# Kernel tuning notes

Measured on AMD Instinct MI355X. Metric: run time of the kernel, lower is better.

## Reference

```python
import jax, jax.numpy as jnp
import numpy as np

EMBED = 384
HEADS = 6
HEAD_SIZE = EMBED // HEADS
EPS = 1e-5


def _layernorm(x, g, b):
    mu = jnp.mean(x, axis=-1, keepdims=True)
    var = jnp.mean(jnp.square(x - mu), axis=-1, keepdims=True)
    return (x - mu) * jax.lax.rsqrt(var + EPS) * g + b


def setup_inputs() -> dict:
    key = jax.random.key(0)
    ks = jax.random.split(key, 16)
    B, T = 64, 256
    s_in = 1.0 / np.sqrt(EMBED)
    return {
        "x": jax.random.normal(ks[0], (B, T, EMBED), dtype=jnp.float32),
        # per-head q/k/v projections, stacked over heads: [H, C, D]
        "Wq": jax.random.normal(ks[1], (HEADS, EMBED, HEAD_SIZE), dtype=jnp.float32) * s_in,
        "bq": jnp.zeros((HEADS, HEAD_SIZE), dtype=jnp.float32),
        "Wk": jax.random.normal(ks[2], (HEADS, EMBED, HEAD_SIZE), dtype=jnp.float32) * s_in,
        "bk": jnp.zeros((HEADS, HEAD_SIZE), dtype=jnp.float32),
        "Wv": jax.random.normal(ks[3], (HEADS, EMBED, HEAD_SIZE), dtype=jnp.float32) * s_in,
        "bv": jnp.zeros((HEADS, HEAD_SIZE), dtype=jnp.float32),
        "Wp": jax.random.normal(ks[4], (EMBED, EMBED), dtype=jnp.float32) * s_in,
        "bp": jnp.zeros((EMBED,), dtype=jnp.float32),
        "W1": jax.random.normal(ks[5], (EMBED, EMBED), dtype=jnp.float32) * s_in,
        "b1": jnp.zeros((EMBED,), dtype=jnp.float32),
        "W2": jax.random.normal(ks[6], (EMBED, EMBED), dtype=jnp.float32) * s_in,
        "b2": jnp.zeros((EMBED,), dtype=jnp.float32),
        "ln1_g": jnp.ones((EMBED,), dtype=jnp.float32),
        "ln1_b": jnp.zeros((EMBED,), dtype=jnp.float32),
        "ln2_g": jnp.ones((EMBED,), dtype=jnp.float32),
        "ln2_b": jnp.zeros((EMBED,), dtype=jnp.float32),
    }


def reference(x, Wq, bq, Wk, bk, Wv, bv, Wp, bp, W1, b1, W2, b2,
              ln1_g, ln1_b, ln2_g, ln2_b):
    B, T, C = x.shape
    h = _layernorm(x, ln1_g, ln1_b)
    # batched per-head projections: [B,H,T,D]
    q = jnp.einsum('btc,hcd->bhtd', h, Wq) + bq[None, :, None, :]
    k = jnp.einsum('btc,hcd->bhtd', h, Wk) + bk[None, :, None, :]
    v = jnp.einsum('btc,hcd->bhtd', h, Wv) + bv[None, :, None, :]
    # NOTE: original scales by embed_size**0.5 (C=384), not head_size.
    wei = jnp.einsum('bhtd,bhsd->bhts', q, k) / jnp.sqrt(jnp.float32(C))
    causal = jnp.tril(jnp.ones((T, T), dtype=bool))
    wei = jnp.where(causal[None, None], wei, -jnp.inf)
    wei = jax.nn.softmax(wei, axis=-1)  # dropout = identity in eval
    attn = jnp.einsum('bhts,bhsd->bhtd', wei, v)  # [B,H,T,D]
    # concat heads in head order -> [B,T,C]
    attn = attn.transpose(0, 2, 1, 3).reshape(B, T, C)
    x = x + attn @ Wp + bp
    h2 = _layernorm(x, ln2_g, ln2_b)
    ff = jax.nn.relu(h2 @ W1 + b1) @ W2 + b2
    return x + ff
```

## Files before the change

### kernel.cpp

```cpp
#include <hip/hip_runtime.h>

typedef _Float16 f16;
typedef _Float16 half8 __attribute__((ext_vector_type(8)));
typedef _Float16 half4v __attribute__((ext_vector_type(4)));
typedef float floatx4 __attribute__((ext_vector_type(4)));

#define B_ 64
#define T_ 256
#define C_ 384
#define H_ 6
#define D_ 64
#define NROWS (B_*T_)

typedef __attribute__((address_space(3))) void lds_void_t;
typedef const __attribute__((address_space(1))) void gvoid_t;

__device__ __forceinline__ void g2lds16(const void* g, void* l) {
  __builtin_amdgcn_global_load_lds((gvoid_t*)g, (lds_void_t*)l, 16, 0, 0);
}

__global__ __launch_bounds__(256) void prep_ln_kernel(
    const float* __restrict__ Wq, const float* __restrict__ Wk, const float* __restrict__ Wv,
    const float* __restrict__ bq, const float* __restrict__ bk, const float* __restrict__ bv,
    const float* __restrict__ Wp, const float* __restrict__ W1, const float* __restrict__ W2,
    f16* __restrict__ Wqkv_t, f16* __restrict__ Wp_t, f16* __restrict__ W1_t, f16* __restrict__ W2_t,
    float* __restrict__ bqkv,
    const float* __restrict__ x, const float* __restrict__ gamma, const float* __restrict__ beta,
    f16* __restrict__ hout)
{
  const int bid = blockIdx.x;
  const int tid = threadIdx.x;
  if (bid >= 217) {
    int row = (bid - 217) * 4 + (tid >> 6);
    int lane = tid & 63;
    const float* xr = x + (size_t)row * 384;
    float v[6]; float s = 0.f;
#pragma unroll
    for (int j = 0; j < 6; j++) { v[j] = xr[lane + 64*j]; s += v[j]; }
#pragma unroll
    for (int m = 1; m < 64; m <<= 1) s += __shfl_xor(s, m);
    float mu = s * (1.f/384.f);
    float var = 0.f;
#pragma unroll
    for (int j = 0; j < 6; j++) { float d = v[j]-mu; var += d*d; }
#pragma unroll
    for (int m = 1; m < 64; m <<= 1) var += __shfl_xor(var, m);
    float rs = rsqrtf(var * (1.f/384.f) + 1e-5f);
    f16* orow = hout + (size_t)row*384;
#pragma unroll
    for (int j = 0; j < 6; j++) {
      int col = lane + 64*j;
      orow[col] = (f16)((v[j]-mu)*rs*gamma[col] + beta[col]);
    }
    return;
  }
  if (bid == 216) {
    for (int i = tid; i < 1152; i += 256) {
      float v;
      if (i < 384)      v = bq[i];
      else if (i < 768) v = bk[i - 384];
      else              v = bv[i - 768];
      bqkv[i] = v;
    }
    return;
  }
  __shared__ __align__(16) float tile[64*68];
  const float* src; int srcStride; f16* dst;
  if (bid < 108) {
    int mat = bid / 36, rem = bid - mat*36;
    int h = rem / 6, kt = rem - h*6;
    const float* W = (mat == 0) ? Wq : (mat == 1) ? Wk : Wv;
    src = W + (size_t)(h*384 + kt*64)*64;
    srcStride = 64;
    dst = Wqkv_t + (size_t)(mat*384 + h*64)*384 + kt*64;
  } else {
    int b2 = bid - 108;
    int mat = b2 / 36, rem = b2 - mat*36;
    int kt = rem / 6, ct = rem - kt*6;
    const float* W = (mat == 0) ? Wp : (mat == 1) ? W1 : W2;
    src = W + (size_t)(kt*64)*384 + ct*64;
    srcStride = 384;
    f16* O = (mat == 0) ? Wp_t : (mat == 1) ? W1_t : W2_t;
    dst = O + (size_t)(ct*64)*384 + kt*64;
  }
#pragma unroll
  for (int i = 0; i < 4; i++) {
    int idx = i*256 + tid;
    int r = idx >> 4, c4 = idx & 15;
    float4 v = *(const float4*)(src + (size_t)r*srcStride + c4*4);
    *(float4*)(&tile[r*68 + c4*4]) = v;
  }
  __syncthreads();
#pragma unroll
  for (int i = 0; i < 4; i++) {
    int idx = i*256 + tid;
    int d = idx >> 4, k4 = idx & 15;
    half4v o;
#pragma unroll
    for (int j = 0; j < 4; j++) o[j] = (f16)tile[(k4*4 + j)*68 + d];
    *(half4v*)(dst + (size_t)d*384 + k4*4) = o;
  }
}

__global__ __launch_bounds__(256) void ln_kernel(const float* __restrict__ x,
    const float* __restrict__ gamma, const float* __restrict__ beta, f16* __restrict__ out)
{
  int row = blockIdx.x * 4 + (threadIdx.x >> 6);
  int lane = threadIdx.x & 63;
  const float* xr = x + (size_t)row * 384;
  float v[6]; float s = 0.f;
#pragma unroll
  for (int j = 0; j < 6; j++) { v[j] = xr[lane + 64*j]; s += v[j]; }
#pragma unroll
  for (int m = 1; m < 64; m <<= 1) s += __shfl_xor(s, m);
  float mu = s * (1.f/384.f);
  float var = 0.f;
#pragma unroll
  for (int j = 0; j < 6; j++) { float d = v[j]-mu; var += d*d; }
#pragma unroll
  for (int m = 1; m < 64; m <<= 1) var += __shfl_xor(var, m);
  float rs = rsqrtf(var * (1.f/384.f) + 1e-5f);
  f16* orow = out + (size_t)row*384;
#pragma unroll
  for (int j = 0; j < 6; j++) {
    int col = lane + 64*j;
    orow[col] = (f16)((v[j]-mu)*rs*gamma[col] + beta[col]);
  }
}

template<int MODE>
__global__ __launch_bounds__(256) void gemm_kernel(
    const f16* __restrict__ A, const f16* __restrict__ Bt,
    const float* __restrict__ bias, const float* __restrict__ res,
    void* __restrict__ outp, int ldo)
{
  __shared__ __align__(16) f16 As[2][128*32];
  __shared__ __align__(16) f16 Bs[2][128*32];
  const int tid = threadIdx.x;
  const int lane = tid & 63, w = tid >> 6;
  const int wm = w >> 1, wn = w & 1;
  const int q = lane >> 4, c15 = lane & 15;
  const long row0 = (long)blockIdx.x * 128;
  const long col0 = (long)blockIdx.y * 128;
  floatx4 acc[4][4] = {};

  const int c0 = tid,        r0c = c0 >> 2, p0 = c0 & 3, g0 = p0 ^ ((r0c >> 1) & 3);
  const int c1 = 256 + tid,  r1c = c1 >> 2, p1 = c1 & 3, g1 = p1 ^ ((r1c >> 1) & 3);
  const f16* Arow0 = A  + (row0 + r0c)*384 + g0*8;
  const f16* Arow1 = A  + (row0 + r1c)*384 + g1*8;
  const f16* Brow0 = Bt + (col0 + r0c)*384 + g0*8;
  const f16* Brow1 = Bt + (col0 + r1c)*384 + g1*8;
  const int dof0 = (w*64)*8, dof1 = (256 + w*64)*8;

  for (int k0 = 0; k0 < 384; k0 += 64) {
#pragma unroll
    for (int hf = 0; hf < 2; hf++) {
      int kk = k0 + hf*32;
      g2lds16(Arow0 + kk, &As[hf][dof0]);
      g2lds16(Arow1 + kk, &As[hf][dof1]);
      g2lds16(Brow0 + kk, &Bs[hf][dof0]);
      g2lds16(Brow1 + kk, &Bs[hf][dof1]);
    }
    __syncthreads();
#pragma unroll
    for (int hf = 0; hf < 2; hf++) {
      half8 af[4], bf[4];
#pragma unroll
      for (int mi = 0; mi < 4; mi++) {
        int r = wm*64 + mi*16 + c15;
        int ph = q ^ ((r >> 1) & 3);
        af[mi] = *(const half8*)(&As[hf][r*32 + ph*8]);
      }
#pragma unroll
      for (int ni = 0; ni < 4; ni++) {
        int r = wn*64 + ni*16 + c15;
        int ph = q ^ ((r >> 1) & 3);
        bf[ni] = *(const half8*)(&Bs[hf][r*32 + ph*8]);
      }
#pragma unroll
      for (int mi = 0; mi < 4; mi++)
#pragma unroll
        for (int ni = 0; ni < 4; ni++)
          acc[mi][ni] = __builtin_amdgcn_mfma_f32_16x16x32_f16(af[mi], bf[ni], acc[mi][ni], 0, 0, 0);
    }
    __syncthreads();
  }

#pragma unroll
  for (int ni = 0; ni < 4; ni++) {
    long col = col0 + wn*64 + ni*16 + c15;
    float bv = bias[col];
#pragma unroll
    for (int mi = 0; mi < 4; mi++) {
      long rowb = row0 + wm*64 + mi*16 + q*4;
#pragma unroll
      for (int r = 0; r < 4; r++) {
        float vo = acc[mi][ni][r] + bv;
        if (MODE == 1) vo = vo > 0.f ? vo : 0.f;
        long o = (rowb + r) * (long)ldo + col;
        if (MODE == 2) {
          ((float*)outp)[o] = vo + res[o];
        } else {
          ((f16*)outp)[o] = (f16)vo;
        }
      }
    }
  }
}

__global__ __launch_bounds__(256, 3) void attn_kernel(const f16* __restrict__ qkv,
                                                      f16* __restrict__ attn_out)
{
  __shared__ __align__(16) char kvbuf[32768];
  __shared__ __align__(16) f16 Pbuf[4][16*128];
  f16* Ks = (f16*)kvbuf;
  unsigned int* vTw = (unsigned int*)kvbuf;
  f16* vT = (f16*)kvbuf;

  const int tid = threadIdx.x;
  const int bid = blockIdx.x;
  const int bh = bid >> 2, qt = bid & 3;
  const int b = bh / 6, h = bh - b*6;
  const f16* qp = qkv + (size_t)b*256*1152 + h*64;
  const f16* kp = qp + 384;
  const f16* vp = qp + 768;
  const int lane = tid & 63, w = tid >> 6;
  const int q = lane >> 4, c15 = lane & 15;

  {
    const int iters = (qt + 1) * 2;
    const int pcbase = w*64 + lane;
    for (int i = 0; i < iters; i++) {
      int pc = i*256 + pcbase;
      int rc = pc >> 3, p = pc & 7;
      int c = p ^ (rc & 7);
      g2lds16(kp + (size_t)rc*1152 + c*8, (char*)kvbuf + (size_t)(i*256 + w*64)*16);
    }
  }
  __syncthreads();

  const int nmax = qt*4 + w;
  const int trow0 = qt*64 + w*16;
  const f16* qrow = qp + (size_t)(trow0 + c15)*1152 + q*8;
  half8 aq0 = *(const half8*)(qrow);
  half8 aq1 = *(const half8*)(qrow + 32);

  floatx4 sacc[16];
#pragma unroll
  for (int ni = 0; ni < 16; ni++) {
    if (ni <= nmax) {
      int s = ni*16 + c15;
      const f16* kr = Ks + s*64;
      int p0 = q ^ (s & 7);
      half8 b0 = *(const half8*)(kr + p0*8);
      half8 b1 = *(const half8*)(kr + (p0 ^ 4)*8);
      floatx4 a = {0.f, 0.f, 0.f, 0.f};
      a = __builtin_amdgcn_mfma_f32_16x16x32_f16(aq0, b0, a, 0, 0, 0);
      a = __builtin_amdgcn_mfma_f32_16x16x32_f16(aq1, b1, a, 0, 0, 0);
      sacc[ni] = a;
    }
  }

  const float scale = 0.051031036307982884f;
  float mx[4] = {-1e30f, -1e30f, -1e30f, -1e30f};
#pragma unroll
  for (int ni = 0; ni < 16; ni++) {
    if (ni < nmax) {
#pragma unroll
      for (int r = 0; r < 4; r++) { float v = sacc[ni][r]*scale; sacc[ni][r] = v; mx[r] = fmaxf(mx[r], v); }
    } else if (ni == nmax) {
#pragma unroll
      for (int r = 0; r < 4; r++) {
        float v = sacc[ni][r]*scale;
        v = (c15 <= q*4 + r) ? v : -1e30f;
        sacc[ni][r] = v; mx[r] = fmaxf(mx[r], v);
      }
    }
  }
#pragma unroll
  for (int r = 0; r < 4; r++) {
    mx[r] = fmaxf(mx[r], __shfl_xor(mx[r], 1));
    mx[r] = fmaxf(mx[r], __shfl_xor(mx[r], 2));
    mx[r] = fmaxf(mx[r], __shfl_xor(mx[r], 4));
    mx[r] = fmaxf(mx[r], __shfl_xor(mx[r], 8));
  }
  float l[4] = {0.f, 0.f, 0.f, 0.f};
#pragma unroll
  for (int ni = 0; ni < 16; ni++) {
    if (ni <= nmax) {
#pragma unroll
      for (int r = 0; r < 4; r++) { float p = __expf(sacc[ni][r] - mx[r]); sacc[ni][r] = p; l[r] += p; }
    }
  }
#pragma unroll
  for (int r = 0; r < 4; r++) {
    l[r] += __shfl_xor(l[r], 1);
    l[r] += __shfl_xor(l[r], 2);
    l[r] += __shfl_xor(l[r], 4);
    l[r] += __shfl_xor(l[r], 8);
  }
  __syncthreads();

  {
    const int iters = qt + 1;
    for (int i = 0; i < iters; i++) {
      int idx = i*256 + tid;
      int sp = idx >> 3, part = idx & 7;
      const f16* v0 = vp + (size_t)(2*sp)*1152 + part*8;
      half8 va = *(const half8*)(v0);
      half8 vb = *(const half8*)(v0 + 1152);
      int csp = sp >> 2, spw = sp & 3;
#pragma unroll
      for (int j = 0; j < 8; j++) {
        int d = part*8 + j;
        int swz = (d & 15) ^ (d >> 3);
        int p = csp ^ swz;
        union { struct { f16 lo, hi; } s; unsigned int u; } pk;
        pk.s.lo = va[j]; pk.s.hi = vb[j];
        vTw[d*128 + p*4 + spw] = pk.u;
      }
    }
  }
  __syncthreads();

  f16* Pw = &Pbuf[w][0];
  floatx4 oacc[4] = {};
  const int kend_w = (nmax + 1) * 16;
#pragma unroll
  for (int ch = 0; ch < 2; ch++) {
    if (ch*128 < kend_w) {
#pragma unroll
      for (int nl = 0; nl < 8; nl++) {
        int ni = ch*8 + nl;
        if (ni <= nmax) {
#pragma unroll
          for (int r = 0; r < 4; r++) {
            int row = q*4 + r;
            int colp = nl*16 + c15;
            int php = (colp >> 3) ^ row;
            Pw[row*128 + php*8 + (colp & 7)] = (f16)sacc[ni][r];
          }
        } else if (ni == nmax + 1) {
#pragma unroll
          for (int r = 0; r < 4; r++) {
            int row = q*4 + r;
            int colp = nl*16 + c15;
            int php = (colp >> 3) ^ row;
            Pw[row*128 + php*8 + (colp & 7)] = (f16)0.f;
          }
        }
      }
#pragma unroll
      for (int kc = 0; kc < 4; kc++) {
        if (ch*128 + kc*32 < kend_w) {
          int pc = (kc*4 + q) ^ c15;
          half8 ap = *(const half8*)(Pw + c15*128 + pc*8);
          int sc = ch*16 + kc*4 + q;
#pragma unroll
          for (int nt = 0; nt < 4; nt++) {
            int d = nt*16 + c15;
            int swz = (d & 15) ^ (d >> 3);
            half8 bv = *(const half8*)(vT + d*256 + ((sc ^ swz))*8);
            oacc[nt] = __builtin_amdgcn_mfma_f32_16x16x32_f16(ap, bv, oacc[nt], 0, 0, 0);
          }
        }
      }
    }
  }

#pragma unroll
  for (int nt = 0; nt < 4; nt++) {
#pragma unroll
    for (int r = 0; r < 4; r++) {
      int t = trow0 + q*4 + r;
      int d = nt*16 + c15;
      attn_out[(size_t)(b*256 + t)*384 + h*64 + d] = (f16)(oacc[nt][r] / l[r]);
    }
  }
}

extern "C" void kernel_launch(void* const* d_in, const int* in_sizes, int n_in,
                              void* d_out, int out_size, void* d_ws, size_t ws_size,
                              hipStream_t stream) {
  const float* x   = (const float*)d_in[0];
  const float* Wq  = (const float*)d_in[1];
  const float* bq  = (const float*)d_in[2];
  const float* Wk  = (const float*)d_in[3];
  const float* bk  = (const float*)d_in[4];
  const float* Wv  = (const float*)d_in[5];
  const float* bv  = (const float*)d_in[6];
  const float* Wp  = (const float*)d_in[7];
  const float* bp  = (const float*)d_in[8];
  const float* W1  = (const float*)d_in[9];
  const float* b1  = (const float*)d_in[10];
  const float* W2  = (const float*)d_in[11];
  const float* b2  = (const float*)d_in[12];
  const float* g1  = (const float*)d_in[13];
  const float* be1 = (const float*)d_in[14];
  const float* g2  = (const float*)d_in[15];
  const float* be2 = (const float*)d_in[16];

  char* ws = (char*)d_ws;
  size_t off = 0;
  auto alloc = [&](size_t bytes) -> void* {
    void* p = ws + off;
    off += (bytes + 255) & ~(size_t)255;
    return p;
  };
  f16*   Wqkv_t = (f16*)  alloc(1152*384*sizeof(f16));
  f16*   Wp_t   = (f16*)  alloc(384*384*sizeof(f16));
  f16*   W1_t   = (f16*)  alloc(384*384*sizeof(f16));
  f16*   W2_t   = (f16*)  alloc(384*384*sizeof(f16));
  float* bqkv   = (float*)alloc(1152*sizeof(float));
  f16*   h      = (f16*)  alloc((size_t)NROWS*384*sizeof(f16));
  f16*   qkv    = (f16*)  alloc((size_t)NROWS*1152*sizeof(f16));
  f16*   attnb  = (f16*)  alloc((size_t)NROWS*384*sizeof(f16));
  float* x2     = (float*)alloc((size_t)NROWS*384*sizeof(float));
  f16*   h2     = (f16*)  alloc((size_t)NROWS*384*sizeof(f16));
  f16*   mid    = (f16*)  alloc((size_t)NROWS*384*sizeof(f16));

  prep_ln_kernel<<<217 + NROWS/4, 256, 0, stream>>>(Wq, Wk, Wv, bq, bk, bv, Wp, W1, W2,
                                                    Wqkv_t, Wp_t, W1_t, W2_t, bqkv,
                                                    x, g1, be1, h);
  gemm_kernel<0><<<dim3(128, 9), 256, 0, stream>>>(h, Wqkv_t, bqkv, nullptr, qkv, 1152);
  attn_kernel<<<B_*H_*4, 256, 0, stream>>>(qkv, attnb);
  gemm_kernel<2><<<dim3(128, 3), 256, 0, stream>>>(attnb, Wp_t, bp, x, x2, 384);
  ln_kernel<<<NROWS/4, 256, 0, stream>>>(x2, g2, be2, h2);
  gemm_kernel<1><<<dim3(128, 3), 256, 0, stream>>>(h2, W1_t, b1, nullptr, mid, 384);
  gemm_kernel<2><<<dim3(128, 3), 256, 0, stream>>>(mid, W2_t, b2, x2, (float*)d_out, 384);
}
```

Measured before the change: 203.8 us.

## Shrink P buffer, prefetch V into registers, raise attention occupancy

The attention kernel halves the per-wave P staging buffer from 128 to 64 columns by processing four 64-key chunks instead of two, and raises launch bounds from 3 to 4 blocks per SM. V rows are now loaded into registers right after the QK^T MFMAs so the global latency overlaps the softmax, and the Q loads are issued before the first barrier. The final normalization multiplies by a reciprocal instead of dividing. Holding up to 8 half8 V registers adds register pressure, which may conflict with the higher occupancy target and cause spills.

After: 203.5 us. Within noise of the previous version (-0.1%).

```diff
diff --git a/kernel.cpp b/kernel.cpp
--- a/kernel.cpp
+++ b/kernel.cpp
@@ -208,11 +208,11 @@
   }
 }
 
-__global__ __launch_bounds__(256, 3) void attn_kernel(const f16* __restrict__ qkv,
+__global__ __launch_bounds__(256, 4) void attn_kernel(const f16* __restrict__ qkv,
                                                       f16* __restrict__ attn_out)
 {
   __shared__ __align__(16) char kvbuf[32768];
-  __shared__ __align__(16) f16 Pbuf[4][16*128];
+  __shared__ __align__(16) f16 Pbuf[4][16*64];
   f16* Ks = (f16*)kvbuf;
   unsigned int* vTw = (unsigned int*)kvbuf;
   f16* vT = (f16*)kvbuf;
@@ -237,13 +237,14 @@
       g2lds16(kp + (size_t)rc*1152 + c*8, (char*)kvbuf + (size_t)(i*256 + w*64)*16);
     }
   }
-  __syncthreads();
 
   const int nmax = qt*4 + w;
   const int trow0 = qt*64 + w*16;
   const f16* qrow = qp + (size_t)(trow0 + c15)*1152 + q*8;
   half8 aq0 = *(const half8*)(qrow);
   half8 aq1 = *(const half8*)(qrow + 32);
+
+  __syncthreads();
 
   floatx4 sacc[16];
 #pragma unroll
@@ -260,6 +261,19 @@
       sacc[ni] = a;
     }
   }
+  __syncthreads();
+
+  half8 va[4], vb[4];
+#pragma unroll
+  for (int i = 0; i < 4; i++) {
+    if (i <= qt) {
+      int idx = i*256 + tid;
+      int sp = idx >> 3, part = idx & 7;
+      const f16* v0 = vp + (size_t)(2*sp)*1152 + part*8;
+      va[i] = *(const half8*)(v0);
+      vb[i] = *(const half8*)(v0 + 1152);
+    }
+  }
 
   const float scale = 0.051031036307982884f;
   float mx[4] = {-1e30f, -1e30f, -1e30f, -1e30f};
@@ -299,16 +313,12 @@
     l[r] += __shfl_xor(l[r], 4);
     l[r] += __shfl_xor(l[r], 8);
   }
-  __syncthreads();
-
-  {
-    const int iters = qt + 1;
-    for (int i = 0; i < iters; i++) {
+
+#pragma unroll
+  for (int i = 0; i < 4; i++) {
+    if (i <= qt) {
       int idx = i*256 + tid;
       int sp = idx >> 3, part = idx & 7;
-      const f16* v0 = vp + (size_t)(2*sp)*1152 + part*8;
-      half8 va = *(const half8*)(v0);
-      half8 vb = *(const half8*)(v0 + 1152);
       int csp = sp >> 2, spw = sp & 3;
 #pragma unroll
       for (int j = 0; j < 8; j++) {
@@ -316,7 +326,7 @@
         int swz = (d & 15) ^ (d >> 3);
         int p = csp ^ swz;
         union { struct { f16 lo, hi; } s; unsigned int u; } pk;
-        pk.s.lo = va[j]; pk.s.hi = vb[j];
+        pk.s.lo = va[i][j]; pk.s.hi = vb[i][j];
         vTw[d*128 + p*4 + spw] = pk.u;
       }
     }
@@ -327,35 +337,35 @@
   floatx4 oacc[4] = {};
   const int kend_w = (nmax + 1) * 16;
 #pragma unroll
-  for (int ch = 0; ch < 2; ch++) {
-    if (ch*128 < kend_w) {
-#pragma unroll
-      for (int nl = 0; nl < 8; nl++) {
-        int ni = ch*8 + nl;
+  for (int ch = 0; ch < 4; ch++) {
+    if (ch*64 < kend_w) {
+#pragma unroll
+      for (int nl = 0; nl < 4; nl++) {
+        int ni = ch*4 + nl;
         if (ni <= nmax) {
 #pragma unroll
           for (int r = 0; r < 4; r++) {
             int row = q*4 + r;
             int colp = nl*16 + c15;
-            int php = (colp >> 3) ^ row;
-            Pw[row*128 + php*8 + (colp & 7)] = (f16)sacc[ni][r];
+            int php = (colp >> 3) ^ (row & 7);
+            Pw[row*64 + php*8 + (colp & 7)] = (f16)sacc[ni][r];
           }
         } else if (ni == nmax + 1) {
 #pragma unroll
           for (int r = 0; r < 4; r++) {
             int row = q*4 + r;
             int colp = nl*16 + c15;
-            int php = (colp >> 3) ^ row;
-            Pw[row*128 + php*8 + (colp & 7)] = (f16)0.f;
+            int php = (colp >> 3) ^ (row & 7);
+            Pw[row*64 + php*8 + (colp & 7)] = (f16)0.f;
           }
         }
       }
 #pragma unroll
-      for (int kc = 0; kc < 4; kc++) {
-        if (ch*128 + kc*32 < kend_w) {
-          int pc = (kc*4 + q) ^ c15;
-          half8 ap = *(const half8*)(Pw + c15*128 + pc*8);
-          int sc = ch*16 + kc*4 + q;
+      for (int kc = 0; kc < 2; kc++) {
+        if (ch*64 + kc*32 < kend_w) {
+          int pc = (kc*4 + q) ^ (c15 & 7);
+          half8 ap = *(const half8*)(Pw + c15*64 + pc*8);
+          int sc = ch*8 + kc*4 + q;
 #pragma unroll
           for (int nt = 0; nt < 4; nt++) {
             int d = nt*16 + c15;
@@ -368,13 +378,16 @@
     }
   }
 
+  float rl[4];
+#pragma unroll
+  for (int r = 0; r < 4; r++) rl[r] = 1.0f / l[r];
 #pragma unroll
   for (int nt = 0; nt < 4; nt++) {
 #pragma unroll
     for (int r = 0; r < 4; r++) {
       int t = trow0 + q*4 + r;
       int d = nt*16 + c15;
-      attn_out[(size_t)(b*256 + t)*384 + h*64 + d] = (f16)(oacc[nt][r] / l[r]);
+      attn_out[(size_t)(b*256 + t)*384 + h*64 + d] = (f16)(oacc[nt][r] * rl[r]);
     }
   }
 }
```
